# Optimization experiments

Measured on AMD Instinct MI355X. Metric: run time of the kernel, lower is better.

## Reference

```python
import jax, jax.numpy as jnp
import numpy as np

N = 50000
E = 800000


def _segment_softmax(logits, seg, n):
    m = jax.ops.segment_max(logits, seg, num_segments=n)
    e = jnp.exp(logits - m[seg])
    s = jax.ops.segment_sum(e, seg, num_segments=n)
    return e / (s[seg] + 1e-16)


def _gin_layer(x, src, dst, w1, b1, w2, b2, n):
    # GINConv, eps=0: mlp(x + sum_{j->i} x_j); MLP = Linear-ReLU-Linear
    agg = jax.ops.segment_sum(x[src], dst, num_segments=n)
    h = x + agg
    h = jnp.maximum(h @ w1 + b1, 0.0)
    return h @ w2 + b2


def _gat_layer(x, src, dst, w, a_src, a_dst, b, n):
    # GATConv heads=1, add_self_loops=True, leaky_relu slope 0.2
    src = jnp.concatenate([src, jnp.arange(n, dtype=src.dtype)])
    dst = jnp.concatenate([dst, jnp.arange(n, dtype=dst.dtype)])
    h = x @ w                                  # [N, D]
    alpha_s = h @ a_src                        # [N]
    alpha_d = h @ a_dst                        # [N]
    logits = jax.nn.leaky_relu(alpha_s[src] + alpha_d[dst], negative_slope=0.2)
    alpha = _segment_softmax(logits, dst, n)   # [E+N]
    out = jax.ops.segment_sum(h[src] * alpha[:, None], dst, num_segments=n)
    return out + b


def setup_inputs() -> dict:
    key = jax.random.key(0)
    ks = jax.random.split(key, 24)

    def w(k, shape, fan_in):
        return (jax.random.normal(k, shape, dtype=jnp.float32) * (1.0 / np.sqrt(fan_in))).astype(jnp.float32)

    inp = {
        "x": jax.random.normal(ks[0], (N, 10), dtype=jnp.float32),
        "edge_index": jax.random.randint(ks[1], (2, E), 0, N, dtype=jnp.int64 if jax.config.jax_enable_x64 else jnp.int32),
        "edge_attr": jax.random.normal(ks[2], (E, 3), dtype=jnp.float32),
        # GIN layer 1: MLP([10, 64, 64])
        "gin1_w1": w(ks[3], (10, 64), 10), "gin1_b1": jnp.zeros((64,), jnp.float32),
        "gin1_w2": w(ks[4], (64, 64), 64), "gin1_b2": jnp.zeros((64,), jnp.float32),
        # GIN layer 2: MLP([64, 128, 128])
        "gin2_w1": w(ks[5], (64, 128), 64), "gin2_b1": jnp.zeros((128,), jnp.float32),
        "gin2_w2": w(ks[6], (128, 128), 128), "gin2_b2": jnp.zeros((128,), jnp.float32),
        # GAT layer 1: 128 -> 256, heads=1
        "gat1_w": w(ks[7], (128, 256), 128),
        "gat1_asrc": w(ks[8], (256,), 256), "gat1_adst": w(ks[9], (256,), 256),
        "gat1_b": jnp.zeros((256,), jnp.float32),
        # GAT layer 2: 256 -> 128, heads=1, concat=False
        "gat2_w": w(ks[10], (256, 128), 256),
        "gat2_asrc": w(ks[11], (128,), 128), "gat2_adst": w(ks[12], (128,), 128),
        "gat2_b": jnp.zeros((128,), jnp.float32),
    }
    return inp


def reference(x, edge_index, edge_attr,
              gin1_w1, gin1_b1, gin1_w2, gin1_b2,
              gin2_w1, gin2_b1, gin2_w2, gin2_b2,
              gat1_w, gat1_asrc, gat1_adst, gat1_b,
              gat2_w, gat2_asrc, gat2_adst, gat2_b):
    src, dst = edge_index[0], edge_index[1]
    n = x.shape[0]
    # edge_attr is accepted but ignored (GINConv does not consume edge features)
    h = _gin_layer(x, src, dst, gin1_w1, gin1_b1, gin1_w2, gin1_b2, n)
    h = jnp.maximum(h, 0.0)
    h = _gin_layer(h, src, dst, gin2_w1, gin2_b1, gin2_w2, gin2_b2, n)
    h = _gat_layer(h, src, dst, gat1_w, gat1_asrc, gat1_adst, gat1_b, n)
    h = jnp.maximum(h, 0.0)
    h = _gat_layer(h, src, dst, gat2_w, gat2_asrc, gat2_adst, gat2_b, n)
    return h
```

## Files before the change

### kernel.cpp

```cpp
#include <hip/hip_runtime.h>
#include <math.h>

__device__ __forceinline__ float lrelu(float x){ return x > 0.f ? x : 0.2f*x; }

typedef short s16x8 __attribute__((ext_vector_type(8)));
typedef float f32x4 __attribute__((ext_vector_type(4)));
typedef unsigned short u16x8 __attribute__((ext_vector_type(8)));

__device__ __forceinline__ f32x4 bmma(s16x8 a, s16x8 b, f32x4 c){
  return __builtin_amdgcn_mfma_f32_16x16x32_bf16(a, b, c, 0, 0, 0);
}

__device__ __forceinline__ unsigned short f2bf(float f){
  unsigned u = __float_as_uint(f);
  unsigned r = (u + 0x7fffu + ((u >> 16) & 1u)) >> 16;
  return (unsigned short)r;
}
__device__ __forceinline__ float bf2f(unsigned short h){
  return __uint_as_float(((unsigned)h) << 16);
}

__global__ void k_deg(const int* __restrict__ dst, int* __restrict__ deg, int E){
  int e = blockIdx.x*blockDim.x + threadIdx.x;
  if(e < E) atomicAdd(&deg[dst[e]], 1);
}

__global__ __launch_bounds__(1024) void k_scan1(const int* __restrict__ deg,
                                                int* __restrict__ part,
                                                int* __restrict__ bsum, int n){
  int i = blockIdx.x*1024 + threadIdx.x;
  int lane = threadIdx.x & 63, wv = threadIdx.x >> 6;
  int v = (i < n) ? deg[i] : 0;
  int s = v;
  #pragma unroll
  for(int off=1; off<64; off<<=1){
    int t = __shfl_up(s, off);
    if(lane >= off) s += t;
  }
  __shared__ int wsum[16];
  if(lane==63) wsum[wv] = s;
  __syncthreads();
  if(wv==0 && lane<16){
    int t = wsum[lane], ss = t;
    #pragma unroll
    for(int off=1; off<16; off<<=1){
      int u = __shfl_up(ss, off);
      if(lane >= off) ss += u;
    }
    wsum[lane] = ss - t;
    if(lane==15) bsum[blockIdx.x] = ss;
  }
  __syncthreads();
  if(i < n) part[i] = s - v + wsum[wv];
}

__global__ __launch_bounds__(1024) void k_scan2(int* __restrict__ bsum, int nb){
  int i = threadIdx.x;
  int lane = i & 63, wv = i >> 6;
  int v = (i < nb) ? bsum[i] : 0;
  int s = v;
  #pragma unroll
  for(int off=1; off<64; off<<=1){
    int t = __shfl_up(s, off);
    if(lane >= off) s += t;
  }
  __shared__ int wsum[16];
  if(lane==63) wsum[wv] = s;
  __syncthreads();
  if(wv==0 && lane<16){
    int t = wsum[lane], ss = t;
    #pragma unroll
    for(int off=1; off<16; off<<=1){
      int u = __shfl_up(ss, off);
      if(lane >= off) ss += u;
    }
    wsum[lane] = ss - t;
  }
  __syncthreads();
  if(i < nb) bsum[i] = s - v + wsum[wv];
}

__global__ void k_scan3(const int* __restrict__ part, const int* __restrict__ bsum,
                        int* __restrict__ offs,
                        float* __restrict__ z0, float* __restrict__ z1,
                        float* __restrict__ z2, float* __restrict__ z3,
                        int n, int E){
  int i = blockIdx.x*blockDim.x + threadIdx.x;
  if(i < n){
    offs[i] = part[i] + bsum[i >> 10];
    z0[i] = 0.f; z1[i] = 0.f; z2[i] = 0.f; z3[i] = 0.f;
  }
  if(i == 0) offs[n] = E;
}

__global__ void k_fill(const int* __restrict__ src, const int* __restrict__ dst,
                       const int* __restrict__ offs, int* __restrict__ cur,
                       int* __restrict__ esrc, int E){
  int e = blockIdx.x*blockDim.x + threadIdx.x;
  if(e < E){
    int d = dst[e];
    int pos = offs[d] + atomicAdd(&cur[d], 1);
    esrc[pos] = src[e];
  }
}

template<bool BR>
__global__ __launch_bounds__(256) void k_gin_agg(const unsigned short* __restrict__ xin,
                                                 const int* __restrict__ offs,
                                                 const int* __restrict__ esrc,
                                                 const float* __restrict__ bias,
                                                 unsigned short* __restrict__ fhi,
                                                 unsigned short* __restrict__ flo, int n){
  int wid  = (int)((blockIdx.x*256u + threadIdx.x) >> 6);
  int lane = threadIdx.x & 63;
  if(wid >= n) return;
  int g = lane >> 3, sub = lane & 7;
  float acc[8];
  #pragma unroll
  for(int k=0;k<8;k++) acc[k] = 0.f;
  int e0 = offs[wid], e1 = offs[wid+1];
  int t = e0;
  for(; t+7 < e1; t += 8){
    int s = esrc[t + g];
    u16x8 r = *(const u16x8*)(xin + (size_t)s*64 + 8*sub);
    #pragma unroll
    for(int k=0;k<8;k++) acc[k] += bf2f(r[k]);
  }
  if(t < e1){
    int idx = t + g;
    bool ok = idx < e1;
    int s = esrc[ok ? idx : e0];
    u16x8 r = *(const u16x8*)(xin + (size_t)s*64 + 8*sub);
    float w = ok ? 1.f : 0.f;
    #pragma unroll
    for(int k=0;k<8;k++) acc[k] += w*bf2f(r[k]);
  }
  #pragma unroll
  for(int off=32; off>=8; off>>=1)
    #pragma unroll
    for(int k=0;k<8;k++) acc[k] += __shfl_down(acc[k], off);
  if(lane < 8){
    u16x8 rs = *(const u16x8*)(xin + (size_t)wid*64 + 8*sub);
    u16x8 h, l;
    #pragma unroll
    for(int k=0;k<8;k++){
      float o = acc[k] + bf2f(rs[k]);
      if(BR) o = fmaxf(o + bias[8*sub + k], 0.f);
      unsigned short hb = f2bf(o);
      h[k] = hb; l[k] = f2bf(o - bf2f(hb));
    }
    int mc = wid >> 4;
    size_t base = ((size_t)(mc*2 + (sub>>2))*64 + (wid & 15) + (sub & 3)*16) * 8;
    *(u16x8*)(fhi + base) = h;
    *(u16x8*)(flo + base) = l;
  }
}

__global__ __launch_bounds__(256) void k_prepA(const float* __restrict__ A,
                                               unsigned short* __restrict__ hi,
                                               unsigned short* __restrict__ lo,
                                               int M, int K, int Mc, int Kc){
  int gid = blockIdx.x*256 + threadIdx.x;
  int lane = gid & 63;
  int fid  = gid >> 6;
  if(fid >= Mc*Kc) return;
  int mc = fid / Kc, kc = fid - mc*Kc;
  int row = mc*16 + (lane & 15);
  int k0  = kc*32 + (lane >> 4)*8;
  s16x8 h, l;
  if(row < M){
    const float* ap = A + (size_t)row*K + k0;
    #pragma unroll
    for(int j=0;j<8;j++){
      float v = (k0 + j < K) ? ap[j] : 0.f;
      unsigned short hb = f2bf(v);
      float r = v - bf2f(hb);
      h[j] = (short)hb; l[j] = (short)f2bf(r);
    }
  } else {
    #pragma unroll
    for(int j=0;j<8;j++){ h[j]=0; l[j]=0; }
  }
  size_t off = (size_t)fid*512 + (size_t)lane*8;
  *(s16x8*)(hi + off) = h;
  *(s16x8*)(lo + off) = l;
}

__global__ __launch_bounds__(256) void k_prepB(const float* __restrict__ B,
                                               unsigned short* __restrict__ hi,
                                               unsigned short* __restrict__ lo,
                                               int K, int Nd, int Kc, int Nc){
  int gid = blockIdx.x*256 + threadIdx.x;
  int lane = gid & 63;
  int fid  = gid >> 6;
  if(fid >= Nc*Kc) return;
  int nc = fid / Kc, kc = fid - nc*Kc;
  int col = nc*16 + (lane & 15);
  int k0  = kc*32 + (lane >> 4)*8;
  s16x8 h, l;
  #pragma unroll
  for(int j=0;j<8;j++){
    int k = k0 + j;
    float v = (k < K) ? B[(size_t)k*Nd + col] : 0.f;
    unsigned short hb = f2bf(v);
    float r = v - bf2f(hb);
    h[j] = (short)hb; l[j] = (short)f2bf(r);
  }
  size_t off = (size_t)fid*512 + (size_t)lane*8;
  *(s16x8*)(hi + off) = h;
  *(s16x8*)(lo + off) = l;
}

template<int ACT, bool HASBIAS, int OMODE>
__global__ __launch_bounds__(256) void k_mgemm(const unsigned short* __restrict__ Ahi,
                                               const unsigned short* __restrict__ Alo,
                                               const unsigned short* __restrict__ Bhi,
                                               const unsigned short* __restrict__ Blo,
                                               const float* __restrict__ bias,
                                               float* __restrict__ C,
                                               unsigned short* __restrict__ Cbf,
                                               unsigned short* __restrict__ foh,
                                               unsigned short* __restrict__ fol,
                                               const float* __restrict__ dwS,
                                               const float* __restrict__ dwD,
                                               float* __restrict__ dotS,
                                               float* __restrict__ dotD,
                                               int M, int Nd, int Kc, int Mc){
  int tid = threadIdx.x;
  int wid = tid >> 6, lane = tid & 63;
  int wm = wid >> 1, wn = wid & 1;
  int mcb = blockIdx.x*8 + wm*4;
  int ncb = blockIdx.y*4 + wn*2;

  f32x4 acc[4][2];
  #pragma unroll
  for(int f=0;f<4;f++)
    #pragma unroll
    for(int g=0;g<2;g++) acc[f][g] = (f32x4){0.f,0.f,0.f,0.f};

  for(int kc=0; kc<Kc; kc++){
    s16x8 ah[4], al[4], bh[2], bl[2];
    #pragma unroll
    for(int f=0;f<4;f++){
      int mcf = mcb + f; if(mcf > Mc-1) mcf = Mc-1;
      size_t off = ((size_t)mcf*Kc + kc)*512 + (size_t)lane*8;
      ah[f] = *(const s16x8*)(Ahi + off);
      al[f] = *(const s16x8*)(Alo + off);
    }
    #pragma unroll
    for(int g=0;g<2;g++){
      size_t off = ((size_t)(ncb+g)*Kc + kc)*512 + (size_t)lane*8;
      bh[g] = *(const s16x8*)(Bhi + off);
      bl[g] = *(const s16x8*)(Blo + off);
    }
    #pragma unroll
    for(int f=0;f<4;f++)
      #pragma unroll
      for(int g=0;g<2;g++){
        acc[f][g] = bmma(ah[f], bh[g], acc[f][g]);
        acc[f][g] = bmma(ah[f], bl[g], acc[f][g]);
        acc[f][g] = bmma(al[f], bh[g], acc[f][g]);
      }
  }

  if constexpr(OMODE <= 1){
    #pragma unroll
    for(int g=0;g<2;g++){
      int col = (ncb+g)*16 + (lane & 15);
      float bv = HASBIAS ? bias[col] : 0.f;
      #pragma unroll
      for(int f=0;f<4;f++){
        int row0 = (mcb+f)*16 + (lane>>4)*4;
        #pragma unroll
        for(int r=0;r<4;r++){
          int row = row0 + r;
          if(row < M){
            float v = acc[f][g][r] + bv;
            if(ACT) v = fmaxf(v, 0.f);
            if(OMODE==1) Cbf[(size_t)row*Nd + col] = f2bf(v);
            else         C  [(size_t)row*Nd + col] = v;
          }
        }
      }
    }
  } else {
    __shared__ float tile[4][64][33];
    #pragma unroll
    for(int g=0;g<2;g++){
      float bv = HASBIAS ? bias[(ncb+g)*16 + (lane&15)] : 0.f;
      int ck = g*16 + (lane & 15);
      #pragma unroll
      for(int f=0;f<4;f++){
        int rb = f*16 + (lane>>4)*4;
        #pragma unroll
        for(int r=0;r<4;r++){
          float v = acc[f][g][r] + bv;
          if(ACT) v = fmaxf(v, 0.f);
          tile[wid][rb + r][ck] = v;
        }
      }
    }
    asm volatile("" ::: "memory");
    int Kcn = Nd >> 5;
    int kcn = ncb >> 1;
    int rr = lane & 15, cb = lane >> 4;
    #pragma unroll
    for(int f=0;f<4;f++){
      int mcf = mcb + f;
      if(mcf >= Mc) continue;
      float o[8];
      #pragma unroll
      for(int j=0;j<8;j++) o[j] = tile[wid][f*16 + rr][cb*8 + j];
      if constexpr(OMODE == 4){
        u16x8 hb;
        #pragma unroll
        for(int j=0;j<8;j++) hb[j] = f2bf(o[j]);
        int row = mcf*16 + rr;
        *(u16x8*)(Cbf + (size_t)row*Nd + kcn*32 + cb*8) = hb;
      } else {
        u16x8 h, l;
        #pragma unroll
        for(int j=0;j<8;j++){
          unsigned short hb = f2bf(o[j]);
          h[j] = hb; l[j] = f2bf(o[j] - bf2f(hb));
        }
        size_t base = ((size_t)mcf*Kcn + kcn)*512 + (size_t)lane*8;
        *(u16x8*)(foh + base) = h;
        *(u16x8*)(fol + base) = l;
      }
      if constexpr(OMODE == 3 || OMODE == 4){
        float sv = 0.f, dv = 0.f;
        #pragma unroll
        for(int j=0;j<8;j++){
          int col = kcn*32 + cb*8 + j;
          sv += o[j]*dwS[col]; dv += o[j]*dwD[col];
        }
        sv += __shfl_xor(sv, 16); sv += __shfl_xor(sv, 32);
        dv += __shfl_xor(dv, 16); dv += __shfl_xor(dv, 32);
        if(cb == 0){
          int row = mcf*16 + rr;
          atomicAdd(dotS + row, sv);
          atomicAdd(dotD + row, dv);
        }
      }
    }
  }
}

template<int L>
__global__ __launch_bounds__(256) void k_wa(const float* __restrict__ W,
                                            const float* __restrict__ a_s, const float* __restrict__ a_d,
                                            float* __restrict__ wa_s, float* __restrict__ wa_d, int rows){
  int wid  = (int)((blockIdx.x*256u + threadIdx.x) >> 6);
  int lane = threadIdx.x & 63;
  if(wid >= rows) return;
  float s = 0.f, d = 0.f;
  #pragma unroll
  for(int j=0;j<L/64;j++){
    int c = lane + j*64;
    float v = W[(size_t)wid*L + c];
    s += v * a_s[c];
    d += v * a_d[c];
  }
  #pragma unroll
  for(int off=32; off; off>>=1){ s += __shfl_down(s, off); d += __shfl_down(d, off); }
  if(lane==0){ wa_s[wid] = s; wa_d[wid] = d; }
}

__global__ __launch_bounds__(256) void k_gat1_aggpre(const unsigned short* __restrict__ hB,
                                                     const float* __restrict__ as_, const float* __restrict__ ad_,
                                                     const int* __restrict__ offs, const int* __restrict__ esrc,
                                                     unsigned short* __restrict__ fhi, unsigned short* __restrict__ flo,
                                                     int n){
  int wid  = (int)((blockIdx.x*256u + threadIdx.x) >> 6);
  int lane = threadIdx.x & 63;
  if(wid >= n) return;
  int q = lane >> 4, sub = lane & 15;
  float adi = ad_[wid];
  u16x8 rs = *(const u16x8*)(hB + (size_t)wid*128 + 8*sub);
  float m, S, acc[8];
  if(q == 0){
    m = lrelu(as_[wid] + adi); S = 1.f;
    #pragma unroll
    for(int k=0;k<8;k++) acc[k] = bf2f(rs[k]);
  } else {
    m = -3e38f; S = 0.f;
    #pragma unroll
    for(int k=0;k<8;k++) acc[k] = 0.f;
  }
  int e0 = offs[wid], e1 = offs[wid+1];
  int t = e0;
  for(; t+7 < e1; t += 8){
    int s0 = esrc[t + q], s1 = esrc[t + 4 + q];
    u16x8 r0 = *(const u16x8*)(hB + (size_t)s0*128 + 8*sub);
    u16x8 r1 = *(const u16x8*)(hB + (size_t)s1*128 + 8*sub);
    float l0 = lrelu(as_[s0] + adi), l1 = lrelu(as_[s1] + adi);
    float lm = fmaxf(l0, l1);
    if(lm > m + 8.f){
      float sc = __expf(m - lm); S *= sc;
      #pragma unroll
      for(int k=0;k<8;k++) acc[k] *= sc;
      m = lm;
    }
    float w0 = __expf(l0 - m), w1 = __expf(l1 - m);
    S += w0 + w1;
    #pragma unroll
    for(int k=0;k<8;k++) acc[k] += w0*bf2f(r0[k]) + w1*bf2f(r1[k]);
  }
  while(t < e1){
    int idx = t + q;
    bool ok = idx < e1;
    int s = esrc[ok ? idx : e0];
    u16x8 r = *(const u16x8*)(hB + (size_t)s*128 + 8*sub);
    float l = ok ? lrelu(as_[s] + adi) : -3e38f;
    if(l > m + 8.f){
      float sc = __expf(m - l); S *= sc;
      #pragma unroll
      for(int k=0;k<8;k++) acc[k] *= sc;
      m = l;
    }
    float w = __expf(l - m);
    S += w;
    #pragma unroll
    for(int k=0;k<8;k++) acc[k] += w*bf2f(r[k]);
    t += 4;
  }
  #pragma unroll
  for(int off=32; off>=16; off>>=1){
    float mo = __shfl_down(m, off), So = __shfl_down(S, off);
    float ao[8];
    #pragma unroll
    for(int k=0;k<8;k++) ao[k] = __shfl_down(acc[k], off);
    float M = fmaxf(m, mo);
    float sc0 = __expf(m - M), sc1 = __expf(mo - M);
    S = S*sc0 + So*sc1;
    #pragma unroll
    for(int k=0;k<8;k++) acc[k] = acc[k]*sc0 + ao[k]*sc1;
    m = M;
  }
  if(lane < 16){
    float inv = 1.f/(S + 1e-16f);
    u16x8 h, l;
    #pragma unroll
    for(int k=0;k<8;k++){
      float v = acc[k]*inv;
      unsigned short hb = f2bf(v);
      h[k] = hb; l[k] = f2bf(v - bf2f(hb));
    }
    int mc = wid >> 4;
    size_t base = ((size_t)(mc*4 + (sub>>2))*64 + (wid & 15) + (sub & 3)*16) * 8;
    *(u16x8*)(fhi + base) = h;
    *(u16x8*)(flo + base) = l;
  }
}

__global__ __launch_bounds__(256) void k_gat2_agg(const unsigned short* __restrict__ hP,
                                                  const float* __restrict__ as_, const float* __restrict__ ad_,
                                                  const int* __restrict__ offs, const int* __restrict__ esrc,
                                                  const float* __restrict__ bias, float* __restrict__ out, int n){
  int wid  = (int)((blockIdx.x*256u + threadIdx.x) >> 6);
  int lane = threadIdx.x & 63;
  if(wid >= n) return;
  int q = lane >> 4, sub = lane & 15;
  float adi = ad_[wid];
  u16x8 rs = *(const u16x8*)(hP + (size_t)wid*128 + 8*sub);
  float m, S, acc[8];
  if(q == 0){
    m = lrelu(as_[wid] + adi); S = 1.f;
    #pragma unroll
    for(int k=0;k<8;k++) acc[k] = bf2f(rs[k]);
  } else {
    m = -3e38f; S = 0.f;
    #pragma unroll
    for(int k=0;k<8;k++) acc[k] = 0.f;
  }
  int e0 = offs[wid], e1 = offs[wid+1];
  int t = e0;
  for(; t+7 < e1; t += 8){
    int s0 = esrc[t + q], s1 = esrc[t + 4 + q];
    u16x8 r0 = *(const u16x8*)(hP + (size_t)s0*128 + 8*sub);
    u16x8 r1 = *(const u16x8*)(hP + (size_t)s1*128 + 8*sub);
    float l0 = lrelu(as_[s0] + adi), l1 = lrelu(as_[s1] + adi);
    float lm = fmaxf(l0, l1);
    if(lm > m + 8.f){
      float sc = __expf(m - lm); S *= sc;
      #pragma unroll
      for(int k=0;k<8;k++) acc[k] *= sc;
      m = lm;
    }
    float w0 = __expf(l0 - m), w1 = __expf(l1 - m);
    S += w0 + w1;
    #pragma unroll
    for(int k=0;k<8;k++) acc[k] += w0*bf2f(r0[k]) + w1*bf2f(r1[k]);
  }
  while(t < e1){
    int idx = t + q;
    bool ok = idx < e1;
    int s = esrc[ok ? idx : e0];
    u16x8 r = *(const u16x8*)(hP + (size_t)s*128 + 8*sub);
    float l = ok ? lrelu(as_[s] + adi) : -3e38f;
    if(l > m + 8.f){
      float sc = __expf(m - l); S *= sc;
      #pragma unroll
      for(int k=0;k<8;k++) acc[k] *= sc;
      m = l;
    }
    float w = __expf(l - m);
    S += w;
    #pragma unroll
    for(int k=0;k<8;k++) acc[k] += w*bf2f(r[k]);
    t += 4;
  }
  #pragma unroll
  for(int off=32; off>=16; off>>=1){
    float mo = __shfl_down(m, off), So = __shfl_down(S, off);
    float ao[8];
    #pragma unroll
    for(int k=0;k<8;k++) ao[k] = __shfl_down(acc[k], off);
    float M = fmaxf(m, mo);
    float sc0 = __expf(m - M), sc1 = __expf(mo - M);
    S = S*sc0 + So*sc1;
    #pragma unroll
    for(int k=0;k<8;k++) acc[k] = acc[k]*sc0 + ao[k]*sc1;
    m = M;
  }
  if(lane < 16){
    float inv = 1.f/(S + 1e-16f);
    float4 o0, o1;
    o0.x = acc[0]*inv + bias[8*sub  ]; o0.y = acc[1]*inv + bias[8*sub+1];
    o0.z = acc[2]*inv + bias[8*sub+2]; o0.w = acc[3]*inv + bias[8*sub+3];
    o1.x = acc[4]*inv + bias[8*sub+4]; o1.y = acc[5]*inv + bias[8*sub+5];
    o1.z = acc[6]*inv + bias[8*sub+6]; o1.w = acc[7]*inv + bias[8*sub+7];
    *(float4*)(out + (size_t)wid*128 + 8*sub)     = o0;
    *(float4*)(out + (size_t)wid*128 + 8*sub + 4) = o1;
  }
}

extern "C" void kernel_launch(void* const* d_in, const int* in_sizes, int n_in,
                              void* d_out, int out_size, void* d_ws, size_t ws_size,
                              hipStream_t stream){
  const float* x        = (const float*)d_in[0];
  const int*   ei       = (const int*)  d_in[1];
  const float* gin1_w1  = (const float*)d_in[3];
  const float* gin1_b1  = (const float*)d_in[4];
  const float* gin1_w2  = (const float*)d_in[5];
  const float* gin1_b2  = (const float*)d_in[6];
  const float* gin2_w1  = (const float*)d_in[7];
  const float* gin2_b1  = (const float*)d_in[8];
  const float* gin2_w2  = (const float*)d_in[9];
  const float* gin2_b2  = (const float*)d_in[10];
  const float* gat1_w   = (const float*)d_in[11];
  const float* gat1_as  = (const float*)d_in[12];
  const float* gat1_ad  = (const float*)d_in[13];
  const float* gat1_b   = (const float*)d_in[14];
  const float* gat2_w   = (const float*)d_in[15];
  const float* gat2_as  = (const float*)d_in[16];
  const float* gat2_ad  = (const float*)d_in[17];
  const float* gat2_b   = (const float*)d_in[18];

  const int n = in_sizes[0] / 10;
  const int E = in_sizes[1] / 2;
  const int* src = ei;
  const int* dst = ei + E;
  const int Mc = (n + 15) / 16;
  const int nb = (n + 1023) / 1024;
  const size_t npad = ((size_t)n*4 + 255) & ~(size_t)255;

  char* w = (char*)d_ws;
  auto carve = [&](size_t bytes)->char*{ char* p = w; w += (bytes + 255) & ~(size_t)255; return p; };
  int*   esrc = (int*)  carve((size_t)E*4);
  int*   offs = (int*)  carve((size_t)(n+1)*4);
  int*   deg  = (int*)  carve(npad);
  int*   cur  = (int*)  carve(npad);
  int*   part = (int*)  carve((size_t)n*4);
  int*   bsum = (int*)  carve((size_t)1024*4);
  unsigned short* Ybf   = (unsigned short*)carve((size_t)n*64*2);
  unsigned short* Hbf   = (unsigned short*)carve((size_t)n*64*2);
  unsigned short* hB2bf = (unsigned short*)carve((size_t)n*128*2);
  unsigned short* Pbf2  = (unsigned short*)carve((size_t)n*128*2);
  float* as_  = (float*)carve((size_t)n*4);
  float* ad_  = (float*)carve((size_t)n*4);
  float* as2_ = (float*)carve((size_t)n*4);
  float* ad2_ = (float*)carve((size_t)n*4);
  float* waS  = (float*)carve(256*4);
  float* waD  = (float*)carve(256*4);
  float* waS2 = (float*)carve(256*4);
  float* waD2 = (float*)carve(256*4);
  unsigned short* FAh = (unsigned short*)carve((size_t)Mc*8*512*2);
  unsigned short* FAl = (unsigned short*)carve((size_t)Mc*8*512*2);
  unsigned short* FBh = (unsigned short*)carve((size_t)Mc*8*512*2);
  unsigned short* FBl = (unsigned short*)carve((size_t)Mc*8*512*2);
  unsigned short* BfH = (unsigned short*)carve((size_t)64*512*2);
  unsigned short* BfL = (unsigned short*)carve((size_t)64*512*2);

  const int TPB = 256;
  int ebk = (E + TPB - 1) / TPB;
  int wbk = (n + 3) / 4;
  int gx  = (Mc + 7) / 8;

  hipMemsetAsync(deg, 0, npad*2, stream);
  k_deg<<<ebk, TPB, 0, stream>>>(dst, deg, E);
  k_scan1<<<nb, 1024, 0, stream>>>(deg, part, bsum, n);
  k_scan2<<<1, 1024, 0, stream>>>(bsum, nb);
  k_scan3<<<(n + 1023)/1024, 1024, 0, stream>>>(part, bsum, offs, as_, ad_, as2_, ad2_, n, E);
  k_fill<<<ebk, TPB, 0, stream>>>(src, dst, offs, cur, esrc, E);

  k_wa<256><<<(128+3)/4, TPB, 0, stream>>>(gat1_w, gat1_as, gat1_ad, waS, waD, 128);
  k_wa<128><<<(256+3)/4, TPB, 0, stream>>>(gat2_w, gat2_as, gat2_ad, waS2, waD2, 256);

  k_prepA<<<(Mc*1*64 + 255)/256, 256, 0, stream>>>(x, FAh, FAl, n, 10, Mc, 1);
  k_prepB<<<(4*1*64 + 255)/256, 256, 0, stream>>>(gin1_w1, BfH, BfL, 10, 64, 1, 4);
  k_mgemm<0,false,1><<<dim3(gx,1), TPB, 0, stream>>>(FAh, FAl, BfH, BfL, nullptr,
      nullptr, Ybf, nullptr, nullptr, nullptr, nullptr, nullptr, nullptr, n, 64, 1, Mc);
  k_gin_agg<true><<<wbk, TPB, 0, stream>>>(Ybf, offs, esrc, gin1_b1, FBh, FBl, n);
  k_prepB<<<(4*2*64 + 255)/256, 256, 0, stream>>>(gin1_w2, BfH, BfL, 64, 64, 2, 4);
  k_mgemm<1,true,1><<<dim3(gx,1), TPB, 0, stream>>>(FBh, FBl, BfH, BfL, gin1_b2,
      nullptr, Hbf, nullptr, nullptr, nullptr, nullptr, nullptr, nullptr, n, 64, 2, Mc);

  k_gin_agg<false><<<wbk, TPB, 0, stream>>>(Hbf, offs, esrc, nullptr, FAh, FAl, n);
  k_prepB<<<(8*2*64 + 255)/256, 256, 0, stream>>>(gin2_w1, BfH, BfL, 64, 128, 2, 8);
  k_mgemm<1,true,2><<<dim3(gx,2), TPB, 0, stream>>>(FAh, FAl, BfH, BfL, gin2_b1,
      nullptr, nullptr, FBh, FBl, nullptr, nullptr, nullptr, nullptr, n, 128, 2, Mc);
  k_prepB<<<(8*4*64 + 255)/256, 256, 0, stream>>>(gin2_w2, BfH, BfL, 128, 128, 4, 8);
  k_mgemm<0,true,4><<<dim3(gx,2), TPB, 0, stream>>>(FBh, FBl, BfH, BfL, gin2_b2,
      nullptr, hB2bf, nullptr, nullptr, waS, waD, as_, ad_, n, 128, 4, Mc);

  k_gat1_aggpre<<<wbk, TPB, 0, stream>>>(hB2bf, as_, ad_, offs, esrc, FAh, FAl, n);
  k_prepB<<<(16*4*64 + 255)/256, 256, 0, stream>>>(gat1_w, BfH, BfL, 128, 256, 4, 16);
  k_mgemm<1,true,3><<<dim3(gx,4), TPB, 0, stream>>>(FAh, FAl, BfH, BfL, gat1_b,
      nullptr, nullptr, FBh, FBl, waS2, waD2, as2_, ad2_, n, 256, 4, Mc);

  k_prepB<<<(8*8*64 + 255)/256, 256, 0, stream>>>(gat2_w, BfH, BfL, 256, 128, 8, 8);
  k_mgemm<0,false,1><<<dim3(gx,2), TPB, 0, stream>>>(FBh, FBl, BfH, BfL, nullptr,
      nullptr, Pbf2, nullptr, nullptr, nullptr, nullptr, nullptr, nullptr, n, 128, 8, Mc);
  k_gat2_agg<<<wbk, TPB, 0, stream>>>(Pbf2, as2_, ad2_, offs, esrc, gat2_b, (float*)d_out, n);
}
```

Before: 343.2 us.

## Batch weight prep into one launch, split CSR fill, unroll aggregation loops by 16

After: 334.1 us. -2.7%, faster.

```diff
diff --git a/kernel.cpp b/kernel.cpp
--- a/kernel.cpp
+++ b/kernel.cpp
@@ -95,12 +95,14 @@
 
 __global__ void k_fill(const int* __restrict__ src, const int* __restrict__ dst,
                        const int* __restrict__ offs, int* __restrict__ cur,
-                       int* __restrict__ esrc, int E){
+                       int* __restrict__ esrc, int E, int lo, int hi){
   int e = blockIdx.x*blockDim.x + threadIdx.x;
   if(e < E){
     int d = dst[e];
-    int pos = offs[d] + atomicAdd(&cur[d], 1);
-    esrc[pos] = src[e];
+    if(d >= lo && d < hi){
+      int pos = offs[d] + atomicAdd(&cur[d], 1);
+      esrc[pos] = src[e];
+    }
   }
 }
 
@@ -120,6 +122,13 @@
   for(int k=0;k<8;k++) acc[k] = 0.f;
   int e0 = offs[wid], e1 = offs[wid+1];
   int t = e0;
+  for(; t+15 < e1; t += 16){
+    int sA = esrc[t + g], sB = esrc[t + 8 + g];
+    u16x8 rA = *(const u16x8*)(xin + (size_t)sA*64 + 8*sub);
+    u16x8 rB = *(const u16x8*)(xin + (size_t)sB*64 + 8*sub);
+    #pragma unroll
+    for(int k=0;k<8;k++) acc[k] += bf2f(rA[k]) + bf2f(rB[k]);
+  }
   for(; t+7 < e1; t += 8){
     int s = esrc[t + g];
     u16x8 r = *(const u16x8*)(xin + (size_t)s*64 + 8*sub);
@@ -186,15 +195,26 @@
   *(s16x8*)(lo + off) = l;
 }
 
-__global__ __launch_bounds__(256) void k_prepB(const float* __restrict__ B,
-                                               unsigned short* __restrict__ hi,
-                                               unsigned short* __restrict__ lo,
-                                               int K, int Nd, int Kc, int Nc){
+__global__ __launch_bounds__(256) void k_prepB_all(const float* __restrict__ B0,
+                                                   const float* __restrict__ B1,
+                                                   const float* __restrict__ B2,
+                                                   const float* __restrict__ B3,
+                                                   const float* __restrict__ B4,
+                                                   const float* __restrict__ B5,
+                                                   unsigned short* __restrict__ hi,
+                                                   unsigned short* __restrict__ lo){
   int gid = blockIdx.x*256 + threadIdx.x;
   int lane = gid & 63;
   int fid  = gid >> 6;
-  if(fid >= Nc*Kc) return;
-  int nc = fid / Kc, kc = fid - nc*Kc;
+  if(fid >= 188) return;
+  const float* B; int K, Nd, Kc, fl;
+  if(fid < 4)       { B=B0; K=10;  Nd=64;  Kc=1; fl=fid;     }
+  else if(fid < 12) { B=B1; K=64;  Nd=64;  Kc=2; fl=fid-4;   }
+  else if(fid < 28) { B=B2; K=64;  Nd=128; Kc=2; fl=fid-12;  }
+  else if(fid < 60) { B=B3; K=128; Nd=128; Kc=4; fl=fid-28;  }
+  else if(fid < 124){ B=B4; K=128; Nd=256; Kc=4; fl=fid-60;  }
+  else              { B=B5; K=256; Nd=128; Kc=8; fl=fid-124; }
+  int nc = fl / Kc, kc = fl - nc*Kc;
   int col = nc*16 + (lane & 15);
   int k0  = kc*32 + (lane >> 4)*8;
   s16x8 h, l;
@@ -347,24 +367,37 @@
   }
 }
 
-template<int L>
-__global__ __launch_bounds__(256) void k_wa(const float* __restrict__ W,
-                                            const float* __restrict__ a_s, const float* __restrict__ a_d,
-                                            float* __restrict__ wa_s, float* __restrict__ wa_d, int rows){
+__global__ __launch_bounds__(256) void k_wa2(const float* __restrict__ W1,
+                                             const float* __restrict__ a1s, const float* __restrict__ a1d,
+                                             const float* __restrict__ W2,
+                                             const float* __restrict__ a2s, const float* __restrict__ a2d,
+                                             float* __restrict__ o1s, float* __restrict__ o1d,
+                                             float* __restrict__ o2s, float* __restrict__ o2d){
   int wid  = (int)((blockIdx.x*256u + threadIdx.x) >> 6);
   int lane = threadIdx.x & 63;
-  if(wid >= rows) return;
   float s = 0.f, d = 0.f;
-  #pragma unroll
-  for(int j=0;j<L/64;j++){
-    int c = lane + j*64;
-    float v = W[(size_t)wid*L + c];
-    s += v * a_s[c];
-    d += v * a_d[c];
-  }
+  if(wid < 128){
+    #pragma unroll
+    for(int j=0;j<4;j++){
+      int c = lane + j*64;
+      float v = W1[(size_t)wid*256 + c];
+      s += v * a1s[c]; d += v * a1d[c];
+    }
+  } else if(wid < 384){
+    int r = wid - 128;
+    #pragma unroll
+    for(int j=0;j<2;j++){
+      int c = lane + j*64;
+      float v = W2[(size_t)r*128 + c];
+      s += v * a2s[c]; d += v * a2d[c];
+    }
+  } else return;
   #pragma unroll
   for(int off=32; off; off>>=1){ s += __shfl_down(s, off); d += __shfl_down(d, off); }
-  if(lane==0){ wa_s[wid] = s; wa_d[wid] = d; }
+  if(lane==0){
+    if(wid < 128){ o1s[wid] = s; o1d[wid] = d; }
+    else         { o2s[wid-128] = s; o2d[wid-128] = d; }
+  }
 }
 
 __global__ __launch_bounds__(256) void k_gat1_aggpre(const unsigned short* __restrict__ hB,
@@ -390,6 +423,27 @@
   }
   int e0 = offs[wid], e1 = offs[wid+1];
   int t = e0;
+  for(; t+15 < e1; t += 16){
+    int s0 = esrc[t + q], s1 = esrc[t + 4 + q], s2 = esrc[t + 8 + q], s3 = esrc[t + 12 + q];
+    u16x8 r0 = *(const u16x8*)(hB + (size_t)s0*128 + 8*sub);
+    u16x8 r1 = *(const u16x8*)(hB + (size_t)s1*128 + 8*sub);
+    u16x8 r2 = *(const u16x8*)(hB + (size_t)s2*128 + 8*sub);
+    u16x8 r3 = *(const u16x8*)(hB + (size_t)s3*128 + 8*sub);
+    float l0 = lrelu(as_[s0] + adi), l1 = lrelu(as_[s1] + adi);
+    float l2 = lrelu(as_[s2] + adi), l3 = lrelu(as_[s3] + adi);
+    float lm = fmaxf(fmaxf(l0, l1), fmaxf(l2, l3));
+    if(lm > m + 8.f){
+      float sc = __expf(m - lm); S *= sc;
+      #pragma unroll
+      for(int k=0;k<8;k++) acc[k] *= sc;
+      m = lm;
+    }
+    float w0 = __expf(l0 - m), w1 = __expf(l1 - m), w2 = __expf(l2 - m), w3 = __expf(l3 - m);
+    S += w0 + w1 + w2 + w3;
+    #pragma unroll
+    for(int k=0;k<8;k++)
+      acc[k] += w0*bf2f(r0[k]) + w1*bf2f(r1[k]) + w2*bf2f(r2[k]) + w3*bf2f(r3[k]);
+  }
   for(; t+7 < e1; t += 8){
     int s0 = esrc[t + q], s1 = esrc[t + 4 + q];
     u16x8 r0 = *(const u16x8*)(hB + (size_t)s0*128 + 8*sub);
@@ -476,6 +530,27 @@
   }
   int e0 = offs[wid], e1 = offs[wid+1];
   int t = e0;
+  for(; t+15 < e1; t += 16){
+    int s0 = esrc[t + q], s1 = esrc[t + 4 + q], s2 = esrc[t + 8 + q], s3 = esrc[t + 12 + q];
+    u16x8 r0 = *(const u16x8*)(hP + (size_t)s0*128 + 8*sub);
+    u16x8 r1 = *(const u16x8*)(hP + (size_t)s1*128 + 8*sub);
+    u16x8 r2 = *(const u16x8*)(hP + (size_t)s2*128 + 8*sub);
+    u16x8 r3 = *(const u16x8*)(hP + (size_t)s3*128 + 8*sub);
+    float l0 = lrelu(as_[s0] + adi), l1 = lrelu(as_[s1] + adi);
+    float l2 = lrelu(as_[s2] + adi), l3 = lrelu(as_[s3] + adi);
+    float lm = fmaxf(fmaxf(l0, l1), fmaxf(l2, l3));
+    if(lm > m + 8.f){
+      float sc = __expf(m - lm); S *= sc;
+      #pragma unroll
+      for(int k=0;k<8;k++) acc[k] *= sc;
+      m = lm;
+    }
+    float w0 = __expf(l0 - m), w1 = __expf(l1 - m), w2 = __expf(l2 - m), w3 = __expf(l3 - m);
+    S += w0 + w1 + w2 + w3;
+    #pragma unroll
+    for(int k=0;k<8;k++)
+      acc[k] += w0*bf2f(r0[k]) + w1*bf2f(r1[k]) + w2*bf2f(r2[k]) + w3*bf2f(r3[k]);
+  }
   for(; t+7 < e1; t += 8){
     int s0 = esrc[t + q], s1 = esrc[t + 4 + q];
     u16x8 r0 = *(const u16x8*)(hP + (size_t)s0*128 + 8*sub);
@@ -590,48 +665,47 @@
   unsigned short* FAl = (unsigned short*)carve((size_t)Mc*8*512*2);
   unsigned short* FBh = (unsigned short*)carve((size_t)Mc*8*512*2);
   unsigned short* FBl = (unsigned short*)carve((size_t)Mc*8*512*2);
-  unsigned short* BfH = (unsigned short*)carve((size_t)64*512*2);
-  unsigned short* BfL = (unsigned short*)carve((size_t)64*512*2);
+  unsigned short* WfH = (unsigned short*)carve((size_t)188*512*2);
+  unsigned short* WfL = (unsigned short*)carve((size_t)188*512*2);
 
   const int TPB = 256;
   int ebk = (E + TPB - 1) / TPB;
   int wbk = (n + 3) / 4;
   int gx  = (Mc + 7) / 8;
+  const size_t W0 = 0, W1o = 4*512, W2o = 12*512, W3o = 28*512, W4o = 60*512, W5o = 124*512;
+
+  k_prepB_all<<<(188*64 + 255)/256, TPB, 0, stream>>>(gin1_w1, gin1_w2, gin2_w1, gin2_w2,
+                                                      gat1_w, gat2_w, WfH, WfL);
+  k_wa2<<<96, TPB, 0, stream>>>(gat1_w, gat1_as, gat1_ad, gat2_w, gat2_as, gat2_ad,
+                                waS, waD, waS2, waD2);
+  k_prepA<<<(Mc*1*64 + 255)/256, 256, 0, stream>>>(x, FAh, FAl, n, 10, Mc, 1);
 
   hipMemsetAsync(deg, 0, npad*2, stream);
   k_deg<<<ebk, TPB, 0, stream>>>(dst, deg, E);
   k_scan1<<<nb, 1024, 0, stream>>>(deg, part, bsum, n);
   k_scan2<<<1, 1024, 0, stream>>>(bsum, nb);
   k_scan3<<<(n + 1023)/1024, 1024, 0, stream>>>(part, bsum, offs, as_, ad_, as2_, ad2_, n, E);
-  k_fill<<<ebk, TPB, 0, stream>>>(src, dst, offs, cur, esrc, E);
-
-  k_wa<256><<<(128+3)/4, TPB, 0, stream>>>(gat1_w, gat1_as, gat1_ad, waS, waD, 128);
-  k_wa<128><<<(256+3)/4, TPB, 0, stream>>>(gat2_w, gat2_as, gat2_ad, waS2, waD2, 256);
-
-  k_prepA<<<(Mc*1*64 + 255)/256, 256, 0, stream>>>(x, FAh, FAl, n, 10, Mc, 1);
-  k_prepB<<<(4*1*64 + 255)/256, 256, 0, stream>>>(gin1_w1, BfH, BfL, 10, 64, 1, 4);
-  k_mgemm<0,false,1><<<dim3(gx,1), TPB, 0, stream>>>(FAh, FAl, BfH, BfL, nullptr,
+  int half = (n + 1) / 2;
+  k_fill<<<ebk, TPB, 0, stream>>>(src, dst, offs, cur, esrc, E, 0, half);
+  k_fill<<<ebk, TPB, 0, stream>>>(src, dst, offs, cur, esrc, E, half, n);
+
+  k_mgemm<0,false,1><<<dim3(gx,1), TPB, 0, stream>>>(FAh, FAl, WfH+W0, WfL+W0, nullptr,
       nullptr, Ybf, nullptr, nullptr, nullptr, nullptr, nullptr, nullptr, n, 64, 1, Mc);
   k_gin_agg<true><<<wbk, TPB, 0, stream>>>(Ybf, offs, esrc, gin1_b1, FBh, FBl, n);
-  k_prepB<<<(4*2*64 + 255)/256, 256, 0, stream>>>(gin1_w2, BfH, BfL, 64, 64, 2, 4);
-  k_mgemm<1,true,1><<<dim3(gx,1), TPB, 0, stream>>>(FBh, FBl, BfH, BfL, gin1_b2,
+  k_mgemm<1,true,1><<<dim3(gx,1), TPB, 0, stream>>>(FBh, FBl, WfH+W1o, WfL+W1o, gin1_b2,
       nullptr, Hbf, nullptr, nullptr, nullptr, nullptr, nullptr, nullptr, n, 64, 2, Mc);
 
   k_gin_agg<false><<<wbk, TPB, 0, stream>>>(Hbf, offs, esrc, nullptr, FAh, FAl, n);
-  k_prepB<<<(8*2*64 + 255)/256, 256, 0, stream>>>(gin2_w1, BfH, BfL, 64, 128, 2, 8);
-  k_mgemm<1,true,2><<<dim3(gx,2), TPB, 0, stream>>>(FAh, FAl, BfH, BfL, gin2_b1,
+  k_mgemm<1,true,2><<<dim3(gx,2), TPB, 0, stream>>>(FAh, FAl, WfH+W2o, WfL+W2o, gin2_b1,
       nullptr, nullptr, FBh, FBl, nullptr, nullptr, nullptr, nullptr, n, 128, 2, Mc);
-  k_prepB<<<(8*4*64 + 255)/256, 256, 0, stream>>>(gin2_w2, BfH, BfL, 128, 128, 4, 8);
-  k_mgemm<0,true,4><<<dim3(gx,2), TPB, 0, stream>>>(FBh, FBl, BfH, BfL, gin2_b2,
+  k_mgemm<0,true,4><<<dim3(gx,2), TPB, 0, stream>>>(FBh, FBl, WfH+W3o, WfL+W3o, gin2_b2,
       nullptr, hB2bf, nullptr, nullptr, waS, waD, as_, ad_, n, 128, 4, Mc);
 
   k_gat1_aggpre<<<wbk, TPB, 0, stream>>>(hB2bf, as_, ad_, offs, esrc, FAh, FAl, n);
-  k_prepB<<<(16*4*64 + 255)/256, 256, 0, stream>>>(gat1_w, BfH, BfL, 128, 256, 4, 16);
-  k_mgemm<1,true,3><<<dim3(gx,4), TPB, 0, stream>>>(FAh, FAl, BfH, BfL, gat1_b,
+  k_mgemm<1,true,3><<<dim3(gx,4), TPB, 0, stream>>>(FAh, FAl, WfH+W4o, WfL+W4o, gat1_b,
       nullptr, nullptr, FBh, FBl, waS2, waD2, as2_, ad2_, n, 256, 4, Mc);
 
-  k_prepB<<<(8*8*64 + 255)/256, 256, 0, stream>>>(gat2_w, BfH, BfL, 256, 128, 8, 8);
-  k_mgemm<0,false,1><<<dim3(gx,2), TPB, 0, stream>>>(FBh, FBl, BfH, BfL, nullptr,
+  k_mgemm<0,false,1><<<dim3(gx,2), TPB, 0, stream>>>(FBh, FBl, WfH+W5o, WfL+W5o, nullptr,
       nullptr, Pbf2, nullptr, nullptr, nullptr, nullptr, nullptr, nullptr, n, 128, 8, Mc);
   k_gat2_agg<<<wbk, TPB, 0, stream>>>(Pbf2, as2_, ad2_, offs, esrc, gat2_b, (float*)d_out, n);
 }
```
